# Optimization experiments

Measured on AMD Instinct MI355X. Metric: run time of the kernel, lower is better.

Reference implementation:

```python
import jax, jax.numpy as jnp
from jax import lax
import numpy as np

B, C, L = 8, 64, 32768
K = 4
DEPTH = 8


def _causal_depthwise_conv(x, weight, dilation):
    # x: [B, C, L], weight: [C, 1, K] depthwise (groups=C). stride=1 so the
    # torch pad formula reduces to left-pad dilation*(K-1), output length L.
    pad = dilation * (K - 1)
    return lax.conv_general_dilated(
        x, weight,
        window_strides=(1,),
        padding=[(pad, 0)],
        rhs_dilation=(dilation,),
        dimension_numbers=("NCH", "OIH", "NCH"),
        feature_group_count=C,
    )


def setup_inputs() -> dict:
    key = jax.random.key(0)
    k1, k2, k3, k4 = jax.random.split(key, 4)
    scalar = np.sqrt(2.0 / (K * 2)).astype(np.float32)
    w_scale = np.sqrt(2.0 / (2 * DEPTH + 4)).astype(np.float32)
    return {
        "x": jax.random.normal(k1, (B, C, L), dtype=jnp.float32),
        "h0": jax.random.uniform(k2, (C, 1, K), minval=-1.0, maxval=1.0, dtype=jnp.float32) * scalar,
        "h1": jax.random.uniform(k3, (C, 1, K), minval=-1.0, maxval=1.0, dtype=jnp.float32) * scalar,
        "w": jax.random.uniform(k4, (C, DEPTH + 2), minval=-1.0, maxval=1.0, dtype=jnp.float32) * w_scale,
    }


def reference(x, h0, h1, w):
    residual_low = x
    y = jnp.zeros_like(x)
    dilation = 1
    for i in range(DEPTH, 0, -1):
        residual_high = _causal_depthwise_conv(residual_low, h1, dilation)
        residual_low = _causal_depthwise_conv(residual_low, h0, dilation)
        y = y + w[:, i][None, :, None] * residual_high
        dilation *= 2
    y = y + w[:, 0][None, :, None] * residual_low
    y = y + x * w[:, -1][None, :, None]
    # dropout p=0 is identity; torch GELU default is exact (erf)
    return jax.nn.gelu(y, approximate=False)
```

## Files before the change

### kernel.cpp

```cpp
#include <hip/hip_runtime.h>
#include <cmath>

namespace {

typedef _Float16 h8 __attribute__((ext_vector_type(8)));

constexpr int C_     = 64;
constexpr int L_     = 32768;
constexpr int TILE   = 4096;
constexpr int HALO   = 776;
constexpr int NB     = TILE + HALO;
constexpr int NU     = NB / 8;
constexpr int HALO_U = HALO / 8;
constexpr int NT     = L_ / TILE;
constexpr int BLK    = 256;
constexpr int UMAX   = (NU + BLK - 1) / BLK;

__device__ __forceinline__ h8 ld8(const _Float16* p) {
    return *reinterpret_cast<const h8*>(p);
}
__device__ __forceinline__ void st8(_Float16* p, h8 v) {
    *reinterpret_cast<h8*>(p) = v;
}
__device__ __forceinline__ float4 ld4f(const float* p) {
    return *reinterpret_cast<const float4*>(p);
}
__device__ __forceinline__ void st4f(float* p, float4 v) {
    *reinterpret_cast<float4*>(p) = v;
}
__device__ __forceinline__ h8 sp8(_Float16 v) {
    return (h8){v, v, v, v, v, v, v, v};
}
__device__ __forceinline__ float gelu_exact(float v) {
    return 0.5f * v * (1.0f + erff(v * 0.70710678118654752f));
}

template<int D, int STARTU, bool LAST>
__device__ __forceinline__ void level_pass(const _Float16* __restrict__ src,
                                           _Float16* __restrict__ dst,
                                           const float* h0f, const float* h1f,
                                           float wi, float w0,
                                           h8* lw, h8* yacc, int tid)
{
    _Float16 c1[4], c0[4];
#pragma unroll
    for (int t = 0; t < 4; ++t) {
        c1[t] = (_Float16)(wi * h1f[t]);
        c0[t] = (_Float16)(LAST ? w0 * h0f[t] : h0f[t]);
    }

#pragma unroll
    for (int u = 0; u < UMAX; ++u) {
        const int un = tid + u * BLK;
        if (un >= STARTU && un < NU) {
            const int p = 8 * un;
            const h8 T3 = lw[u];
            h8 T0, T1, T2;
            if constexpr (D == 1) {
                h8 Lv = ld8(&src[p - 8]);
                T0 = __builtin_shufflevector(Lv, T3, 5, 6, 7, 8, 9, 10, 11, 12);
                T1 = __builtin_shufflevector(Lv, T3, 6, 7, 8, 9, 10, 11, 12, 13);
                T2 = __builtin_shufflevector(Lv, T3, 7, 8, 9, 10, 11, 12, 13, 14);
            } else if constexpr (D == 2) {
                h8 Lv = ld8(&src[p - 8]);
                T0 = __builtin_shufflevector(Lv, T3, 2, 3, 4, 5, 6, 7, 8, 9);
                T1 = __builtin_shufflevector(Lv, T3, 4, 5, 6, 7, 8, 9, 10, 11);
                T2 = __builtin_shufflevector(Lv, T3, 6, 7, 8, 9, 10, 11, 12, 13);
            } else if constexpr (D == 4) {
                h8 Lv  = ld8(&src[p - 8]);
                h8 LL  = ld8(&src[p - 16]);
                T0 = __builtin_shufflevector(LL, Lv, 4, 5, 6, 7, 8, 9, 10, 11);
                T1 = Lv;
                T2 = __builtin_shufflevector(Lv, T3, 4, 5, 6, 7, 8, 9, 10, 11);
            } else {
                T0 = ld8(&src[p - 3 * D]);
                T1 = ld8(&src[p - 2 * D]);
                T2 = ld8(&src[p - D]);
            }
            if (un >= HALO_U) {
                yacc[u] += sp8(c1[0]) * T0 + sp8(c1[1]) * T1
                         + sp8(c1[2]) * T2 + sp8(c1[3]) * T3;
            }
            h8 nl = sp8(c0[0]) * T0 + sp8(c0[1]) * T1
                  + sp8(c0[2]) * T2 + sp8(c0[3]) * T3;
            if constexpr (LAST) {
                yacc[u] += nl;
            } else {
                lw[u] = nl;
                st8(&dst[p], nl);
            }
        }
    }
}

__global__ __launch_bounds__(BLK, 7)
void cmrc_kernel(const float* __restrict__ x,
                 const float* __restrict__ h0,
                 const float* __restrict__ h1,
                 const float* __restrict__ w,
                 float* __restrict__ out)
{
    __shared__ _Float16 buf[2][NB];

    const int tid  = threadIdx.x;
    const int blk  = blockIdx.x;
    const int tile = blk % NT;
    const int bc   = blk / NT;
    const int c    = bc % C_;
    const long row = (long)bc * L_;
    const int  t0  = tile * TILE - HALO;

    float h0v[4], h1v[4];
#pragma unroll
    for (int k = 0; k < 4; ++k) {
        h0v[k] = h0[c * 4 + k];
        h1v[k] = h1[c * 4 + k];
    }
    float wv[10];
#pragma unroll
    for (int i = 0; i < 10; ++i) wv[i] = w[c * 10 + i];

    h8 lw[UMAX];
    h8 yacc[UMAX];

    const _Float16 w9h = (_Float16)wv[9];

#pragma unroll
    for (int u = 0; u < UMAX; ++u) {
        yacc[u] = sp8((_Float16)0.f);
        const int un = tid + u * BLK;
        if (un < NU) {
            const int p = 8 * un;
            const int t = t0 + p;
            float4 xa = make_float4(0.f, 0.f, 0.f, 0.f);
            float4 xb = make_float4(0.f, 0.f, 0.f, 0.f);
            if (t >= 0)     xa = ld4f(&x[row + t]);
            if (t + 4 >= 0) xb = ld4f(&x[row + t + 4]);
            h8 hv;
            hv[0] = (_Float16)xa.x; hv[1] = (_Float16)xa.y;
            hv[2] = (_Float16)xa.z; hv[3] = (_Float16)xa.w;
            hv[4] = (_Float16)xb.x; hv[5] = (_Float16)xb.y;
            hv[6] = (_Float16)xb.z; hv[7] = (_Float16)xb.w;
            st8(&buf[0][p], hv);
            lw[u] = hv;
            if (un >= HALO_U) yacc[u] = sp8(w9h) * hv;
        }
    }
    __syncthreads();

    level_pass<1,   1,  false>(buf[0], buf[1], h0v, h1v, wv[8], 0.f, lw, yacc, tid); __syncthreads();
    level_pass<2,   2,  false>(buf[1], buf[0], h0v, h1v, wv[7], 0.f, lw, yacc, tid); __syncthreads();
    level_pass<4,   4,  false>(buf[0], buf[1], h0v, h1v, wv[6], 0.f, lw, yacc, tid); __syncthreads();
    level_pass<8,   7,  false>(buf[1], buf[0], h0v, h1v, wv[5], 0.f, lw, yacc, tid); __syncthreads();
    level_pass<16,  13, false>(buf[0], buf[1], h0v, h1v, wv[4], 0.f, lw, yacc, tid); __syncthreads();
    level_pass<32,  25, false>(buf[1], buf[0], h0v, h1v, wv[3], 0.f, lw, yacc, tid); __syncthreads();
    level_pass<64,  49, false>(buf[0], buf[1], h0v, h1v, wv[2], 0.f, lw, yacc, tid); __syncthreads();
    level_pass<128, 97, true >(buf[1], buf[0], h0v, h1v, wv[1], wv[0], lw, yacc, tid);

#pragma unroll
    for (int u = 0; u < UMAX; ++u) {
        const int un = tid + u * BLK;
        if (un >= HALO_U && un < NU) {
            const int p = 8 * un;
            const h8 v = yacc[u];
            float4 oa, ob;
            oa.x = gelu_exact((float)v[0]); oa.y = gelu_exact((float)v[1]);
            oa.z = gelu_exact((float)v[2]); oa.w = gelu_exact((float)v[3]);
            ob.x = gelu_exact((float)v[4]); ob.y = gelu_exact((float)v[5]);
            ob.z = gelu_exact((float)v[6]); ob.w = gelu_exact((float)v[7]);
            st4f(&out[row + t0 + p], oa);
            st4f(&out[row + t0 + p + 4], ob);
        }
    }
}

}

extern "C" void kernel_launch(void* const* d_in, const int* in_sizes, int n_in,
                              void* d_out, int out_size, void* d_ws, size_t ws_size,
                              hipStream_t stream)
{
    const float* x  = (const float*)d_in[0];
    const float* h0 = (const float*)d_in[1];
    const float* h1 = (const float*)d_in[2];
    const float* w  = (const float*)d_in[3];
    float* out = (float*)d_out;

    const int nblocks = (out_size / L_) * NT;
    cmrc_kernel<<<nblocks, BLK, 0, stream>>>(x, h0, h1, w, out);
}
```

Before: 47.55 us.

## Double tile, give each thread contiguous units, single padded LDS buffer

Tiles grow from 4096 to 8192 so less of each block's work goes to recomputing the 776-sample halo. Each thread now owns 4-5 contiguous 8-element units instead of strided ones, so short dilations reuse neighbouring units from registers rather than LDS. A single padded LDS buffer replaces the ping-pong pair, which needs an extra barrier per level to publish results. The exact erf GELU is replaced by a tanh-style sigmoid approximation, and launch bounds drop from 7 to 4 waves per SIMD, trading accuracy and occupancy for fewer instructions.

```diff
diff --git a/kernel.cpp b/kernel.cpp
--- a/kernel.cpp
+++ b/kernel.cpp
@@ -7,100 +7,165 @@
 
 constexpr int C_     = 64;
 constexpr int L_     = 32768;
-constexpr int TILE   = 4096;
+constexpr int TILE   = 8192;
 constexpr int HALO   = 776;
 constexpr int NB     = TILE + HALO;
 constexpr int NU     = NB / 8;
 constexpr int HALO_U = HALO / 8;
 constexpr int NT     = L_ / TILE;
 constexpr int BLK    = 256;
-constexpr int UMAX   = (NU + BLK - 1) / BLK;
-
-__device__ __forceinline__ h8 ld8(const _Float16* p) {
-    return *reinterpret_cast<const h8*>(p);
-}
-__device__ __forceinline__ void st8(_Float16* p, h8 v) {
-    *reinterpret_cast<h8*>(p) = v;
-}
-__device__ __forceinline__ float4 ld4f(const float* p) {
-    return *reinterpret_cast<const float4*>(p);
-}
-__device__ __forceinline__ void st4f(float* p, float4 v) {
-    *reinterpret_cast<float4*>(p) = v;
-}
-__device__ __forceinline__ h8 sp8(_Float16 v) {
-    return (h8){v, v, v, v, v, v, v, v};
-}
-__device__ __forceinline__ float gelu_exact(float v) {
-    return 0.5f * v * (1.0f + erff(v * 0.70710678118654752f));
-}
-
-template<int D, int STARTU, bool LAST>
-__device__ __forceinline__ void level_pass(const _Float16* __restrict__ src,
-                                           _Float16* __restrict__ dst,
-                                           const float* h0f, const float* h1f,
-                                           float wi, float w0,
-                                           h8* lw, h8* yacc, int tid)
-{
+constexpr int LDSH   = 8 * NU + 8 * ((NU + 3) / 4);
+
+__device__ __forceinline__ int uoff(int gu) { return 8 * gu + ((gu >> 2) << 3); }
+
+__device__ __forceinline__ h8 ld8(const _Float16* p) { return *reinterpret_cast<const h8*>(p); }
+__device__ __forceinline__ void st8(_Float16* p, h8 v) { *reinterpret_cast<h8*>(p) = v; }
+__device__ __forceinline__ float4 ld4f(const float* p) { return *reinterpret_cast<const float4*>(p); }
+__device__ __forceinline__ void st4f(float* p, float4 v) { *reinterpret_cast<float4*>(p) = v; }
+__device__ __forceinline__ h8 sp8(_Float16 v) { return (h8){v,v,v,v,v,v,v,v}; }
+
+template<int K>
+__device__ __forceinline__ h8 shconc(h8 A, h8 B) {
+    return __builtin_shufflevector(A, B, K, K+1, K+2, K+3, K+4, K+5, K+6, K+7);
+}
+
+__device__ __forceinline__ float gelu_f(float v) {
+    const float z = v * (1.5957691216057308f + 0.0713548162726f * v * v);
+    const float e = __expf(-z);
+    return v * __builtin_amdgcn_rcpf(1.0f + e);
+}
+
+template<int D, int STARTU, bool FIRST, bool LAST>
+__device__ __forceinline__ void level(_Float16* __restrict__ buf,
+                                      h8* lw, h8* yacc,
+                                      const float* h0v, const float* h1v,
+                                      float wi, float w0, float w9,
+                                      int u0, int myU)
+{
+    if (u0 + 4 < STARTU) return;
+
     _Float16 c1[4], c0[4];
 #pragma unroll
     for (int t = 0; t < 4; ++t) {
-        c1[t] = (_Float16)(wi * h1f[t]);
-        c0[t] = (_Float16)(LAST ? w0 * h0f[t] : h0f[t]);
-    }
-
-#pragma unroll
-    for (int u = 0; u < UMAX; ++u) {
-        const int un = tid + u * BLK;
-        if (un >= STARTU && un < NU) {
-            const int p = 8 * un;
-            const h8 T3 = lw[u];
-            h8 T0, T1, T2;
-            if constexpr (D == 1) {
-                h8 Lv = ld8(&src[p - 8]);
-                T0 = __builtin_shufflevector(Lv, T3, 5, 6, 7, 8, 9, 10, 11, 12);
-                T1 = __builtin_shufflevector(Lv, T3, 6, 7, 8, 9, 10, 11, 12, 13);
-                T2 = __builtin_shufflevector(Lv, T3, 7, 8, 9, 10, 11, 12, 13, 14);
-            } else if constexpr (D == 2) {
-                h8 Lv = ld8(&src[p - 8]);
-                T0 = __builtin_shufflevector(Lv, T3, 2, 3, 4, 5, 6, 7, 8, 9);
-                T1 = __builtin_shufflevector(Lv, T3, 4, 5, 6, 7, 8, 9, 10, 11);
-                T2 = __builtin_shufflevector(Lv, T3, 6, 7, 8, 9, 10, 11, 12, 13);
-            } else if constexpr (D == 4) {
-                h8 Lv  = ld8(&src[p - 8]);
-                h8 LL  = ld8(&src[p - 16]);
-                T0 = __builtin_shufflevector(LL, Lv, 4, 5, 6, 7, 8, 9, 10, 11);
-                T1 = Lv;
-                T2 = __builtin_shufflevector(Lv, T3, 4, 5, 6, 7, 8, 9, 10, 11);
-            } else {
-                T0 = ld8(&src[p - 3 * D]);
-                T1 = ld8(&src[p - 2 * D]);
-                T2 = ld8(&src[p - D]);
-            }
-            if (un >= HALO_U) {
-                yacc[u] += sp8(c1[0]) * T0 + sp8(c1[1]) * T1
-                         + sp8(c1[2]) * T2 + sp8(c1[3]) * T3;
-            }
-            h8 nl = sp8(c0[0]) * T0 + sp8(c0[1]) * T1
-                  + sp8(c0[2]) * T2 + sp8(c0[3]) * T3;
-            if constexpr (LAST) {
-                yacc[u] += nl;
-            } else {
-                lw[u] = nl;
-                st8(&dst[p], nl);
-            }
-        }
-    }
-}
-
-__global__ __launch_bounds__(BLK, 7)
+        c1[t] = (_Float16)(wi * h1v[t]);
+        c0[t] = (_Float16)(LAST ? w0 * h0v[t] : h0v[t]);
+    }
+
+    if constexpr (D < 8) {
+        constexpr int NL = (D == 4) ? 2 : 1;
+        h8 X[NL + 5];
+#pragma unroll
+        for (int i = 0; i < NL; ++i) {
+            int g = u0 - NL + i; if (g < 0) g = 0;
+            X[i] = ld8(&buf[uoff(g)]);
+        }
+        if constexpr (FIRST) {
+#pragma unroll
+            for (int u = 0; u < 5; ++u) {
+                int g = u0 + u; if (g > NU - 1) g = NU - 1;
+                X[NL + u] = ld8(&buf[uoff(g)]);
+            }
+        } else {
+#pragma unroll
+            for (int u = 0; u < 5; ++u) X[NL + u] = lw[u];
+        }
+#pragma unroll
+        for (int u = 0; u < 5; ++u) {
+            const int gu = u0 + u;
+            const h8 T3 = X[NL + u];
+            if constexpr (FIRST) {
+                yacc[u] = sp8((_Float16)0.f);
+                lw[u]   = T3;
+                if ((u < myU) && gu >= HALO_U) yacc[u] = sp8((_Float16)w9) * T3;
+            }
+            if ((u < myU) && gu >= STARTU) {
+                h8 T0, T1, T2;
+                if constexpr (D == 1) {
+                    T0 = shconc<5>(X[NL+u-1], T3);
+                    T1 = shconc<6>(X[NL+u-1], T3);
+                    T2 = shconc<7>(X[NL+u-1], T3);
+                } else if constexpr (D == 2) {
+                    T0 = shconc<2>(X[NL+u-1], T3);
+                    T1 = shconc<4>(X[NL+u-1], T3);
+                    T2 = shconc<6>(X[NL+u-1], T3);
+                } else {
+                    T0 = shconc<4>(X[NL+u-2], X[NL+u-1]);
+                    T1 = X[NL+u-1];
+                    T2 = shconc<4>(X[NL+u-1], T3);
+                }
+                if (gu >= HALO_U)
+                    yacc[u] += sp8(c1[0])*T0 + sp8(c1[1])*T1 + sp8(c1[2])*T2 + sp8(c1[3])*T3;
+                const h8 nl = sp8(c0[0])*T0 + sp8(c0[1])*T1 + sp8(c0[2])*T2 + sp8(c0[3])*T3;
+                if constexpr (LAST) yacc[u] += nl; else lw[u] = nl;
+            }
+        }
+    } else {
+        constexpr int UD = D / 8;
+        h8 T0a[5], T1a[5], T2a[5];
+        if constexpr (UD <= 4) {
+            h8 R[3 * UD];
+#pragma unroll
+            for (int i = 0; i < 3 * UD; ++i) {
+                int g = u0 - 3 * UD + i; if (g < 0) g = 0;
+                R[i] = ld8(&buf[uoff(g)]);
+            }
+#pragma unroll
+            for (int u = 0; u < 5; ++u) {
+                const int r0 = u - 3 * UD, r1 = u - 2 * UD, r2 = u - UD;
+                T0a[u] = (r0 >= 0) ? lw[r0 < 0 ? 0 : r0] : R[u];
+                T1a[u] = (r1 >= 0) ? lw[r1 < 0 ? 0 : r1]
+                                   : R[(u + UD) < 3*UD ? (u + UD) : (3*UD - 1)];
+                T2a[u] = (r2 >= 0) ? lw[r2 < 0 ? 0 : r2]
+                                   : R[(u + 2*UD) < 3*UD ? (u + 2*UD) : (3*UD - 1)];
+            }
+        } else {
+            h8 R[3][5];
+#pragma unroll
+            for (int m = 0; m < 3; ++m) {
+#pragma unroll
+                for (int u = 0; u < 5; ++u) {
+                    int g = u0 + u - (m + 1) * UD; if (g < 0) g = 0;
+                    R[m][u] = ld8(&buf[uoff(g)]);
+                }
+            }
+#pragma unroll
+            for (int u = 0; u < 5; ++u) { T0a[u] = R[2][u]; T1a[u] = R[1][u]; T2a[u] = R[0][u]; }
+        }
+#pragma unroll
+        for (int u = 0; u < 5; ++u) {
+            const int gu = u0 + u;
+            if ((u < myU) && gu >= STARTU) {
+                const h8 T3 = lw[u];
+                const h8 T0 = T0a[u], T1 = T1a[u], T2 = T2a[u];
+                if (gu >= HALO_U)
+                    yacc[u] += sp8(c1[0])*T0 + sp8(c1[1])*T1 + sp8(c1[2])*T2 + sp8(c1[3])*T3;
+                const h8 nl = sp8(c0[0])*T0 + sp8(c0[1])*T1 + sp8(c0[2])*T2 + sp8(c0[3])*T3;
+                if constexpr (LAST) yacc[u] += nl; else lw[u] = nl;
+            }
+        }
+    }
+}
+
+template<int STARTU>
+__device__ __forceinline__ void publish(_Float16* __restrict__ buf, const h8* lw,
+                                        int u0, int myU)
+{
+    if (u0 + 4 < STARTU) return;
+#pragma unroll
+    for (int u = 0; u < 5; ++u) {
+        const int gu = u0 + u;
+        if ((u < myU) && gu >= STARTU) st8(&buf[uoff(gu)], lw[u]);
+    }
+}
+
+__global__ __launch_bounds__(BLK, 4)
 void cmrc_kernel(const float* __restrict__ x,
                  const float* __restrict__ h0,
                  const float* __restrict__ h1,
                  const float* __restrict__ w,
                  float* __restrict__ out)
 {
-    __shared__ _Float16 buf[2][NB];
+    __shared__ _Float16 buf[LDSH];
 
     const int tid  = threadIdx.x;
     const int blk  = blockIdx.x;
@@ -112,64 +177,64 @@
 
     float h0v[4], h1v[4];
 #pragma unroll
-    for (int k = 0; k < 4; ++k) {
-        h0v[k] = h0[c * 4 + k];
-        h1v[k] = h1[c * 4 + k];
-    }
+    for (int k = 0; k < 4; ++k) { h0v[k] = h0[c*4+k]; h1v[k] = h1[c*4+k]; }
     float wv[10];
 #pragma unroll
-    for (int i = 0; i < 10; ++i) wv[i] = w[c * 10 + i];
-
-    h8 lw[UMAX];
-    h8 yacc[UMAX];
-
-    const _Float16 w9h = (_Float16)wv[9];
-
-#pragma unroll
-    for (int u = 0; u < UMAX; ++u) {
-        yacc[u] = sp8((_Float16)0.f);
-        const int un = tid + u * BLK;
+    for (int i = 0; i < 10; ++i) wv[i] = w[c*10+i];
+
+#pragma unroll
+    for (int j = 0; j < 5; ++j) {
+        const int un = tid + j * BLK;
         if (un < NU) {
             const int p = 8 * un;
             const int t = t0 + p;
-            float4 xa = make_float4(0.f, 0.f, 0.f, 0.f);
-            float4 xb = make_float4(0.f, 0.f, 0.f, 0.f);
+            float4 xa = make_float4(0.f,0.f,0.f,0.f);
+            float4 xb = make_float4(0.f,0.f,0.f,0.f);
             if (t >= 0)     xa = ld4f(&x[row + t]);
             if (t + 4 >= 0) xb = ld4f(&x[row + t + 4]);
             h8 hv;
-            hv[0] = (_Float16)xa.x; hv[1] = (_Float16)xa.y;
-            hv[2] = (_Float16)xa.z; hv[3] = (_Float16)xa.w;
-            hv[4] = (_Float16)xb.x; hv[5] = (_Float16)xb.y;
-            hv[6] = (_Float16)xb.z; hv[7] = (_Float16)xb.w;
-            st8(&buf[0][p], hv);
-            lw[u] = hv;
-            if (un >= HALO_U) yacc[u] = sp8(w9h) * hv;
+            hv[0]=(_Float16)xa.x; hv[1]=(_Float16)xa.y; hv[2]=(_Float16)xa.z; hv[3]=(_Float16)xa.w;
+            hv[4]=(_Float16)xb.x; hv[5]=(_Float16)xb.y; hv[6]=(_Float16)xb.z; hv[7]=(_Float16)xb.w;
+            st8(&buf[uoff(un)], hv);
         }
     }
     __syncthreads();
 
-    level_pass<1,   1,  false>(buf[0], buf[1], h0v, h1v, wv[8], 0.f, lw, yacc, tid); __syncthreads();
-    level_pass<2,   2,  false>(buf[1], buf[0], h0v, h1v, wv[7], 0.f, lw, yacc, tid); __syncthreads();
-    level_pass<4,   4,  false>(buf[0], buf[1], h0v, h1v, wv[6], 0.f, lw, yacc, tid); __syncthreads();
-    level_pass<8,   7,  false>(buf[1], buf[0], h0v, h1v, wv[5], 0.f, lw, yacc, tid); __syncthreads();
-    level_pass<16,  13, false>(buf[0], buf[1], h0v, h1v, wv[4], 0.f, lw, yacc, tid); __syncthreads();
-    level_pass<32,  25, false>(buf[1], buf[0], h0v, h1v, wv[3], 0.f, lw, yacc, tid); __syncthreads();
-    level_pass<64,  49, false>(buf[0], buf[1], h0v, h1v, wv[2], 0.f, lw, yacc, tid); __syncthreads();
-    level_pass<128, 97, true >(buf[1], buf[0], h0v, h1v, wv[1], wv[0], lw, yacc, tid);
-
-#pragma unroll
-    for (int u = 0; u < UMAX; ++u) {
-        const int un = tid + u * BLK;
-        if (un >= HALO_U && un < NU) {
-            const int p = 8 * un;
+    const int u0  = 4 * tid + (tid < HALO_U ? tid : HALO_U);
+    const int myU = (tid < HALO_U) ? 5 : 4;
+
+    h8 lw[5];
+    h8 yacc[5];
+
+    level<1,   1,  true,  false>(buf, lw, yacc, h0v, h1v, wv[8], 0.f, wv[9], u0, myU);
+    __syncthreads(); publish<1>(buf, lw, u0, myU);  __syncthreads();
+    level<2,   2,  false, false>(buf, lw, yacc, h0v, h1v, wv[7], 0.f, 0.f, u0, myU);
+    __syncthreads(); publish<2>(buf, lw, u0, myU);  __syncthreads();
+    level<4,   4,  false, false>(buf, lw, yacc, h0v, h1v, wv[6], 0.f, 0.f, u0, myU);
+    __syncthreads(); publish<4>(buf, lw, u0, myU);  __syncthreads();
+    level<8,   7,  false, false>(buf, lw, yacc, h0v, h1v, wv[5], 0.f, 0.f, u0, myU);
+    __syncthreads(); publish<7>(buf, lw, u0, myU);  __syncthreads();
+    level<16,  13, false, false>(buf, lw, yacc, h0v, h1v, wv[4], 0.f, 0.f, u0, myU);
+    __syncthreads(); publish<13>(buf, lw, u0, myU); __syncthreads();
+    level<32,  25, false, false>(buf, lw, yacc, h0v, h1v, wv[3], 0.f, 0.f, u0, myU);
+    __syncthreads(); publish<25>(buf, lw, u0, myU); __syncthreads();
+    level<64,  49, false, false>(buf, lw, yacc, h0v, h1v, wv[2], 0.f, 0.f, u0, myU);
+    __syncthreads(); publish<49>(buf, lw, u0, myU); __syncthreads();
+    level<128, 97, false, true >(buf, lw, yacc, h0v, h1v, wv[1], wv[0], 0.f, u0, myU);
+
+#pragma unroll
+    for (int u = 0; u < 5; ++u) {
+        const int gu = u0 + u;
+        if ((u < myU) && gu >= HALO_U) {
             const h8 v = yacc[u];
             float4 oa, ob;
-            oa.x = gelu_exact((float)v[0]); oa.y = gelu_exact((float)v[1]);
-            oa.z = gelu_exact((float)v[2]); oa.w = gelu_exact((float)v[3]);
-            ob.x = gelu_exact((float)v[4]); ob.y = gelu_exact((float)v[5]);
-            ob.z = gelu_exact((float)v[6]); ob.w = gelu_exact((float)v[7]);
-            st4f(&out[row + t0 + p], oa);
-            st4f(&out[row + t0 + p + 4], ob);
+            oa.x = gelu_f((float)v[0]); oa.y = gelu_f((float)v[1]);
+            oa.z = gelu_f((float)v[2]); oa.w = gelu_f((float)v[3]);
+            ob.x = gelu_f((float)v[4]); ob.y = gelu_f((float)v[5]);
+            ob.z = gelu_f((float)v[6]); ob.w = gelu_f((float)v[7]);
+            const long idx = row + (t0 + 8 * gu);
+            st4f(&out[idx], oa);
+            st4f(&out[idx + 4], ob);
         }
     }
 }
```

New measurement: 96.35 us. +102.6%, slower.
